# Optimization experiments

Hardware: AMD Instinct MI355X
Metric: run time of the kernel (lower is better)

## Reference

```python
import jax, jax.numpy as jnp
import numpy as np

N_IN = 128
N_BASIS = 16


def setup_inputs() -> dict:
    key = jax.random.key(0)
    ks = jax.random.split(key, 6)
    N, P = 50000, 200000
    prop = jax.random.normal(ks[0], (N, N_IN), dtype=jnp.float32)
    idx_i = jax.random.randint(ks[1], (P,), 0, N, dtype=jnp.int64)
    idx_j = jax.random.randint(ks[2], (P,), 0, N, dtype=jnp.int64)
    basis = jax.random.normal(ks[3], (P, N_BASIS), dtype=jnp.float32)
    # bias-free MLP: n_in=128 -> hidden 256 (tanh) -> n_out=2048
    W1 = jax.random.normal(ks[4], (N_IN, 256), dtype=jnp.float32) * (1.0 / np.sqrt(N_IN))
    W2 = jax.random.normal(ks[5], (256, N_IN * N_BASIS), dtype=jnp.float32) * (1.0 / np.sqrt(256))
    return {"prop": prop, "idx_i": idx_i, "idx_j": idx_j, "basis": basis, "W1": W1, "W2": W2}


def reference(prop, idx_i, idx_j, basis, W1, W2):
    # gather node features at edge endpoints and sum
    inter = prop[idx_i] + prop[idx_j]              # [P, n_in]
    # bias-free MLP with tanh on hidden layer
    h = jnp.tanh(inter @ W1)                       # [P, 256]
    h = h @ W2                                     # [P, n_in * n_basis]
    # contract with per-edge basis: 'pcb,pb->pc'
    h = h.reshape(-1, N_IN, N_BASIS)               # [P, n_in, n_basis]
    out = jnp.einsum('pcb,pb->pc', h, basis)       # [P, n_in]
    return out[:, None, :]                         # [P, 1, n_in]
```

## Files before the change

kernel.cpp:

```cpp
#include <hip/hip_runtime.h>

#define N_IN 128
#define HID 256
#define NB 16
#define BM 128
#define HS_STRIDE 264
#define BS_STRIDE 17

typedef __attribute__((ext_vector_type(8))) short s8v;
typedef __attribute__((ext_vector_type(4))) float f4v;

__device__ __forceinline__ unsigned short f2bf(float f) {
  unsigned int u = __float_as_uint(f);
  u += 0x7fffu + ((u >> 16) & 1u);
  return (unsigned short)(u >> 16);
}

__device__ __forceinline__ float tanh_fast(float x) {
  float e = __expf(2.0f * x);
  return 1.0f - 2.0f * __builtin_amdgcn_rcpf(e + 1.0f);
}

__global__ void __launch_bounds__(256)
prep2_kernel(const float* __restrict__ W1, const float* __restrict__ W2,
             unsigned short* __restrict__ W1f, unsigned short* __restrict__ W2f) {
  __shared__ unsigned short T[32 * 1024];

  const int t = threadIdx.x;
  const int lane = t & 63;
  const int wv = t >> 6;
  const int l15 = lane & 15;
  const int l4 = lane >> 4;
  const int bid = blockIdx.x;

  if (bid < 16) {
    const int kk = bid >> 1, ch = bid & 1;
    const float* src = W2 + (long)(kk * 32) * (N_IN * NB) + ch * 1024;
#pragma unroll
    for (int it = 0; it < 32; ++it) {
      int idx = it * 256 + t;
      int r = idx >> 8;
      int c4 = idx & 255;
      f4v v = __builtin_nontemporal_load((const f4v*)(src + r * (N_IN * NB) + c4 * 4));
      unsigned short* d = &T[r * 1024 + c4 * 4];
      d[0] = f2bf(v[0]); d[1] = f2bf(v[1]); d[2] = f2bf(v[2]); d[3] = f2bf(v[3]);
    }
    __syncthreads();
#pragma unroll
    for (int fi = 0; fi < 16; ++fi) {
      int f = fi * 4 + wv;
      int b = f >> 2, ctl = f & 3;
      int colb = ctl * 256 + l15 * 16 + b;
      s8v v;
#pragma unroll
      for (int j = 0; j < 8; ++j)
        v[j] = (short)T[(l4 * 8 + j) * 1024 + colb];
      *(s8v*)(W2f + ((((b * 8 + kk) * 8 + (ch * 4 + ctl)) * 64 + lane) << 3)) = v;
    }
  } else if (bid < 20) {
    const int kk = bid - 16;
    const float* src = W1 + (long)(kk * 32) * HID;
#pragma unroll
    for (int it = 0; it < 8; ++it) {
      int idx = it * 256 + t;
      int r = idx >> 6;
      int c4 = idx & 63;
      f4v v = __builtin_nontemporal_load((const f4v*)(src + r * HID + c4 * 4));
      unsigned short* d = &T[r * 256 + c4 * 4];
      d[0] = f2bf(v[0]); d[1] = f2bf(v[1]); d[2] = f2bf(v[2]); d[3] = f2bf(v[3]);
    }
    __syncthreads();
#pragma unroll
    for (int fi = 0; fi < 4; ++fi) {
      int f = fi * 4 + wv;
      int pass = f >> 3, ct = f & 7;
      int col = pass * 128 + ct * 16 + l15;
      s8v v;
#pragma unroll
      for (int j = 0; j < 8; ++j)
        v[j] = (short)T[(l4 * 8 + j) * 256 + col];
      *(s8v*)(W1f + ((((pass * 4 + kk) * 8 + ct) * 64 + lane) << 3)) = v;
    }
  }
}

__global__ void __launch_bounds__(256, 2)
pilayer_kernel(const float* __restrict__ prop,
               const int* __restrict__ idx_i,
               const int* __restrict__ idx_j,
               const float* __restrict__ basis,
               const unsigned short* __restrict__ W1f,
               const unsigned short* __restrict__ W2f,
               float* __restrict__ out, int P) {
  __shared__ unsigned short Hs[BM * HS_STRIDE];
  __shared__ float basisS[BM * BS_STRIDE];

  const int t = threadIdx.x;
  const int lane = t & 63;
  const int wv = t >> 6;
  const int l15 = lane & 15;
  const int l4 = lane >> 4;
  const int tile0 = blockIdx.x * BM;
  const int row0 = wv * 32;

  int pidx[2], qidx[2];
#pragma unroll
  for (int rt = 0; rt < 2; ++rt) {
    int p = tile0 + row0 + rt * 16 + l15; if (p >= P) p = P - 1;
    pidx[rt] = idx_i[p];
    qidx[rt] = idx_j[p];
  }

  {
    int r = t >> 1;
    int c0 = (t & 1) * 8;
    int p = tile0 + r; if (p >= P) p = P - 1;
    const f4v* bp = (const f4v*)(basis + (long)p * NB + c0);
    f4v b0 = __builtin_nontemporal_load(bp);
    f4v b1 = __builtin_nontemporal_load(bp + 1);
    float* dst = &basisS[r * BS_STRIDE + c0];
    dst[0] = b0[0]; dst[1] = b0[1]; dst[2] = b0[2]; dst[3] = b0[3];
    dst[4] = b1[0]; dst[5] = b1[1]; dst[6] = b1[2]; dst[7] = b1[3];
  }

  {
    s8v afr[4][2];
#pragma unroll
    for (int kk = 0; kk < 4; ++kk) {
      int k0 = kk * 32 + l4 * 8;
#pragma unroll
      for (int rt = 0; rt < 2; ++rt) {
        const float4* ai = (const float4*)(prop + (long)pidx[rt] * N_IN + k0);
        const float4* aj = (const float4*)(prop + (long)qidx[rt] * N_IN + k0);
        float4 x0 = ai[0], x1 = ai[1];
        float4 y0 = aj[0], y1 = aj[1];
        s8v a;
        a[0] = (short)f2bf(x0.x + y0.x); a[1] = (short)f2bf(x0.y + y0.y);
        a[2] = (short)f2bf(x0.z + y0.z); a[3] = (short)f2bf(x0.w + y0.w);
        a[4] = (short)f2bf(x1.x + y1.x); a[5] = (short)f2bf(x1.y + y1.y);
        a[6] = (short)f2bf(x1.z + y1.z); a[7] = (short)f2bf(x1.w + y1.w);
        afr[kk][rt] = a;
      }
    }
#pragma unroll
    for (int pass = 0; pass < 2; ++pass) {
      f4v acc[2][8];
#pragma unroll
      for (int rt = 0; rt < 2; ++rt)
#pragma unroll
        for (int ct = 0; ct < 8; ++ct) acc[rt][ct] = (f4v){0.f, 0.f, 0.f, 0.f};
#pragma unroll
      for (int kk = 0; kk < 4; ++kk) {
#pragma unroll
        for (int ct = 0; ct < 8; ++ct) {
          s8v bfr = *(const s8v*)(W1f + ((((pass * 4 + kk) * 8 + ct) * 64 + lane) << 3));
#pragma unroll
          for (int rt = 0; rt < 2; ++rt)
            acc[rt][ct] = __builtin_amdgcn_mfma_f32_16x16x32_bf16(afr[kk][rt], bfr, acc[rt][ct], 0, 0, 0);
        }
      }
#pragma unroll
      for (int rt = 0; rt < 2; ++rt)
#pragma unroll
        for (int ct = 0; ct < 8; ++ct)
#pragma unroll
          for (int r = 0; r < 4; ++r) {
            int lrow = row0 + rt * 16 + l4 * 4 + r;
            int col = pass * 128 + ct * 16 + l15;
            Hs[lrow * HS_STRIDE + col] = f2bf(tanh_fast(acc[rt][ct][r]));
          }
    }
  }

  __syncthreads();

  const int rg = wv >> 1, cg = wv & 1;
  const int rbase = rg * 64;

  f4v o[4][4];
#pragma unroll
  for (int rt = 0; rt < 4; ++rt)
#pragma unroll
    for (int q = 0; q < 4; ++q) o[rt][q] = (f4v){0.f, 0.f, 0.f, 0.f};

#pragma unroll 1
  for (int khalf = 0; khalf < 2; ++khalf) {
    s8v areg[4][4];
#pragma unroll
    for (int rt = 0; rt < 4; ++rt)
#pragma unroll
      for (int kloc = 0; kloc < 4; ++kloc)
        areg[rt][kloc] = *(const s8v*)&Hs[(rbase + rt * 16 + l15) * HS_STRIDE +
                                          (khalf * 4 + kloc) * 32 + l4 * 8];

    s8v bf[4][4];
#pragma unroll
    for (int q0 = 0; q0 < 3; ++q0)
#pragma unroll
      for (int kloc = 0; kloc < 4; ++kloc)
        bf[q0][kloc] = *(const s8v*)(W2f +
            ((((khalf * 4 + kloc) * 8) + cg * 4 + q0) << 9) + lane * 8);

#pragma unroll 1
    for (int b = 0; b < 16; ++b) {
      float bs[4][4];
#pragma unroll
      for (int rt = 0; rt < 4; ++rt)
#pragma unroll
        for (int r = 0; r < 4; ++r)
          bs[rt][r] = basisS[(rbase + rt * 16 + l4 * 4 + r) * BS_STRIDE + b];

#pragma unroll
      for (int q = 0; q < 4; ++q) {
        {
          int nb = b + ((q + 3) >> 2); if (nb > 15) nb = 15;
          int nq = (q + 3) & 3;
#pragma unroll
          for (int kloc = 0; kloc < 4; ++kloc)
            bf[(q + 3) & 3][kloc] = *(const s8v*)(W2f +
                (((nb * 8 + khalf * 4 + kloc) * 8 + cg * 4 + nq) << 9) + lane * 8);
        }
        f4v g[4];
#pragma unroll
        for (int rt = 0; rt < 4; ++rt) g[rt] = (f4v){0.f, 0.f, 0.f, 0.f};
        __builtin_amdgcn_s_setprio(1);
#pragma unroll
        for (int kloc = 0; kloc < 4; ++kloc)
#pragma unroll
          for (int rt = 0; rt < 4; ++rt)
            g[rt] = __builtin_amdgcn_mfma_f32_16x16x32_bf16(areg[rt][kloc], bf[q][kloc], g[rt], 0, 0, 0);
        __builtin_amdgcn_s_setprio(0);
#pragma unroll
        for (int rt = 0; rt < 4; ++rt)
#pragma unroll
          for (int r = 0; r < 4; ++r)
            o[rt][q][r] += g[rt][r] * bs[rt][r];
      }
    }
  }

#pragma unroll
  for (int rt = 0; rt < 4; ++rt)
#pragma unroll
    for (int r = 0; r < 4; ++r) {
      int p = tile0 + rbase + rt * 16 + l4 * 4 + r;
      if (p < P) {
        float* op = out + (long)p * N_IN + cg * 64 + l15;
#pragma unroll
        for (int q = 0; q < 4; ++q)
          __builtin_nontemporal_store(o[rt][q][r], op + q * 16);
      }
    }
}

extern "C" void kernel_launch(void* const* d_in, const int* in_sizes, int n_in,
                              void* d_out, int out_size, void* d_ws, size_t ws_size,
                              hipStream_t stream) {
  const float* prop  = (const float*)d_in[0];
  const int* idx_i   = (const int*)d_in[1];
  const int* idx_j   = (const int*)d_in[2];
  const float* basis = (const float*)d_in[3];
  const float* W1    = (const float*)d_in[4];
  const float* W2    = (const float*)d_in[5];
  float* out = (float*)d_out;
  int P = in_sizes[1];

  unsigned short* W1f = (unsigned short*)d_ws;
  unsigned short* W2f = W1f + N_IN * HID;

  prep2_kernel<<<20, 256, 0, stream>>>(W1, W2, W1f, W2f);

  int ntiles = (P + BM - 1) / BM;
  pilayer_kernel<<<ntiles, 256, 0, stream>>>(prop, idx_i, idx_j, basis, W1f, W2f, out, P);
}
```

Before: 336.6 us.

## Switch second GEMM to 32x32x16 MFMA with repacked W2 and transposed basis

```diff
diff --git a/kernel.cpp b/kernel.cpp
--- a/kernel.cpp
+++ b/kernel.cpp
@@ -5,10 +5,10 @@
 #define NB 16
 #define BM 128
 #define HS_STRIDE 264
-#define BS_STRIDE 17
 
 typedef __attribute__((ext_vector_type(8))) short s8v;
 typedef __attribute__((ext_vector_type(4))) float f4v;
+typedef __attribute__((ext_vector_type(16))) float f16v;
 
 __device__ __forceinline__ unsigned short f2bf(float f) {
   unsigned int u = __float_as_uint(f);
@@ -22,43 +22,43 @@
 }
 
 __global__ void __launch_bounds__(256)
-prep2_kernel(const float* __restrict__ W1, const float* __restrict__ W2,
+prep4_kernel(const float* __restrict__ W1, const float* __restrict__ W2,
              unsigned short* __restrict__ W1f, unsigned short* __restrict__ W2f) {
-  __shared__ unsigned short T[32 * 1024];
+  __shared__ unsigned short T[8192];
 
   const int t = threadIdx.x;
   const int lane = t & 63;
   const int wv = t >> 6;
   const int l15 = lane & 15;
-  const int l4 = lane >> 4;
+  const int l31 = lane & 31;
+  const int l4 = (lane >> 4) & 3;
+  const int hi = lane >> 5;
   const int bid = blockIdx.x;
 
-  if (bid < 16) {
-    const int kk = bid >> 1, ch = bid & 1;
-    const float* src = W2 + (long)(kk * 32) * (N_IN * NB) + ch * 1024;
-#pragma unroll
-    for (int it = 0; it < 32; ++it) {
+  if (bid < 64) {
+    const int ks = bid >> 2, CT = bid & 3;
+    const float* src = W2 + (long)(ks * 16) * (N_IN * NB) + CT * 512;
+#pragma unroll
+    for (int it = 0; it < 8; ++it) {
       int idx = it * 256 + t;
-      int r = idx >> 8;
-      int c4 = idx & 255;
+      int r = idx >> 7;
+      int c4 = idx & 127;
       f4v v = __builtin_nontemporal_load((const f4v*)(src + r * (N_IN * NB) + c4 * 4));
-      unsigned short* d = &T[r * 1024 + c4 * 4];
+      unsigned short* d = &T[r * 512 + c4 * 4];
       d[0] = f2bf(v[0]); d[1] = f2bf(v[1]); d[2] = f2bf(v[2]); d[3] = f2bf(v[3]);
     }
     __syncthreads();
 #pragma unroll
-    for (int fi = 0; fi < 16; ++fi) {
-      int f = fi * 4 + wv;
-      int b = f >> 2, ctl = f & 3;
-      int colb = ctl * 256 + l15 * 16 + b;
+    for (int fi = 0; fi < 4; ++fi) {
+      int b = fi * 4 + wv;
       s8v v;
 #pragma unroll
       for (int j = 0; j < 8; ++j)
-        v[j] = (short)T[(l4 * 8 + j) * 1024 + colb];
-      *(s8v*)(W2f + ((((b * 8 + kk) * 8 + (ch * 4 + ctl)) * 64 + lane) << 3)) = v;
-    }
-  } else if (bid < 20) {
-    const int kk = bid - 16;
+        v[j] = (short)T[(hi * 8 + j) * 512 + l31 * 16 + b];
+      *(s8v*)(W2f + ((((b * 16 + ks) * 4 + CT) * 64 + lane) << 3)) = v;
+    }
+  } else if (bid < 68) {
+    const int kk = bid - 64;
     const float* src = W1 + (long)(kk * 32) * HID;
 #pragma unroll
     for (int it = 0; it < 8; ++it) {
@@ -93,13 +93,15 @@
                const unsigned short* __restrict__ W2f,
                float* __restrict__ out, int P) {
   __shared__ unsigned short Hs[BM * HS_STRIDE];
-  __shared__ float basisS[BM * BS_STRIDE];
+  __shared__ float basisT[NB * BM];
 
   const int t = threadIdx.x;
   const int lane = t & 63;
   const int wv = t >> 6;
   const int l15 = lane & 15;
-  const int l4 = lane >> 4;
+  const int l31 = lane & 31;
+  const int l4 = (lane >> 4) & 3;
+  const int hi = lane >> 5;
   const int tile0 = blockIdx.x * BM;
   const int row0 = wv * 32;
 
@@ -118,9 +120,11 @@
     const f4v* bp = (const f4v*)(basis + (long)p * NB + c0);
     f4v b0 = __builtin_nontemporal_load(bp);
     f4v b1 = __builtin_nontemporal_load(bp + 1);
-    float* dst = &basisS[r * BS_STRIDE + c0];
-    dst[0] = b0[0]; dst[1] = b0[1]; dst[2] = b0[2]; dst[3] = b0[3];
-    dst[4] = b1[0]; dst[5] = b1[1]; dst[6] = b1[2]; dst[7] = b1[3];
+#pragma unroll
+    for (int u = 0; u < 4; ++u) {
+      basisT[(c0 + u) * BM + r] = b0[u];
+      basisT[(c0 + 4 + u) * BM + r] = b1[u];
+    }
   }
 
   {
@@ -177,78 +181,89 @@
   const int rg = wv >> 1, cg = wv & 1;
   const int rbase = rg * 64;
 
-  f4v o[4][4];
-#pragma unroll
-  for (int rt = 0; rt < 4; ++rt)
-#pragma unroll
-    for (int q = 0; q < 4; ++q) o[rt][q] = (f4v){0.f, 0.f, 0.f, 0.f};
+  f16v o[2][2];
+#pragma unroll
+  for (int rt2 = 0; rt2 < 2; ++rt2)
+#pragma unroll
+    for (int ct = 0; ct < 2; ++ct)
+#pragma unroll
+      for (int e = 0; e < 16; ++e) o[rt2][ct][e] = 0.f;
+
+  s8v bf[2][4];
 
 #pragma unroll 1
   for (int khalf = 0; khalf < 2; ++khalf) {
-    s8v areg[4][4];
-#pragma unroll
-    for (int rt = 0; rt < 4; ++rt)
-#pragma unroll
-      for (int kloc = 0; kloc < 4; ++kloc)
-        areg[rt][kloc] = *(const s8v*)&Hs[(rbase + rt * 16 + l15) * HS_STRIDE +
-                                          (khalf * 4 + kloc) * 32 + l4 * 8];
-
-    s8v bf[4][4];
-#pragma unroll
-    for (int q0 = 0; q0 < 3; ++q0)
-#pragma unroll
-      for (int kloc = 0; kloc < 4; ++kloc)
-        bf[q0][kloc] = *(const s8v*)(W2f +
-            ((((khalf * 4 + kloc) * 8) + cg * 4 + q0) << 9) + lane * 8);
+    s8v areg[2][8];
+#pragma unroll
+    for (int rt2 = 0; rt2 < 2; ++rt2)
+#pragma unroll
+      for (int ksl = 0; ksl < 8; ++ksl)
+        areg[rt2][ksl] = *(const s8v*)&Hs[(rbase + rt2 * 32 + l31) * HS_STRIDE +
+                                          khalf * 128 + ksl * 16 + hi * 8];
+
+#pragma unroll
+    for (int kl = 0; kl < 4; ++kl) {
+      int ks = khalf * 8 + kl;
+      bf[0][kl] = *(const s8v*)(W2f + ((((0 * 16 + ks) * 4 + cg * 2 + 0) * 64 + lane) << 3));
+    }
 
 #pragma unroll 1
     for (int b = 0; b < 16; ++b) {
-      float bs[4][4];
-#pragma unroll
-      for (int rt = 0; rt < 4; ++rt)
-#pragma unroll
-        for (int r = 0; r < 4; ++r)
-          bs[rt][r] = basisS[(rbase + rt * 16 + l4 * 4 + r) * BS_STRIDE + b];
-
-#pragma unroll
-      for (int q = 0; q < 4; ++q) {
-        {
-          int nb = b + ((q + 3) >> 2); if (nb > 15) nb = 15;
-          int nq = (q + 3) & 3;
-#pragma unroll
-          for (int kloc = 0; kloc < 4; ++kloc)
-            bf[(q + 3) & 3][kloc] = *(const s8v*)(W2f +
-                (((nb * 8 + khalf * 4 + kloc) * 8 + cg * 4 + nq) << 9) + lane * 8);
+      f4v bsv[2][4];
+#pragma unroll
+      for (int rt2 = 0; rt2 < 2; ++rt2)
+#pragma unroll
+        for (int q4 = 0; q4 < 4; ++q4)
+          bsv[rt2][q4] = *(const f4v*)&basisT[b * BM + rbase + rt2 * 32 + q4 * 8 + hi * 4];
+
+#pragma unroll
+      for (int ct = 0; ct < 2; ++ct) {
+        f16v g[2];
+#pragma unroll
+        for (int rt2 = 0; rt2 < 2; ++rt2)
+#pragma unroll
+          for (int e = 0; e < 16; ++e) g[rt2][e] = 0.f;
+
+#pragma unroll
+        for (int kc = 0; kc < 2; ++kc) {
+          {
+            int nb = b, nct = ct, nkc = kc ^ 1;
+            if (kc == 1) { nct = ct ^ 1; if (ct == 1) { nb = b + 1; if (nb > 15) nb = 15; } nkc = 0; }
+#pragma unroll
+            for (int kl = 0; kl < 4; ++kl) {
+              int ks = khalf * 8 + nkc * 4 + kl;
+              bf[kc ^ 1][kl] = *(const s8v*)(W2f +
+                  ((((nb * 16 + ks) * 4 + cg * 2 + nct) * 64 + lane) << 3));
+            }
+          }
+          __builtin_amdgcn_s_setprio(1);
+#pragma unroll
+          for (int kl = 0; kl < 4; ++kl)
+#pragma unroll
+            for (int rt2 = 0; rt2 < 2; ++rt2)
+              g[rt2] = __builtin_amdgcn_mfma_f32_32x32x16_bf16(areg[rt2][kc * 4 + kl],
+                                                               bf[kc][kl], g[rt2], 0, 0, 0);
+          __builtin_amdgcn_s_setprio(0);
         }
-        f4v g[4];
-#pragma unroll
-        for (int rt = 0; rt < 4; ++rt) g[rt] = (f4v){0.f, 0.f, 0.f, 0.f};
-        __builtin_amdgcn_s_setprio(1);
-#pragma unroll
-        for (int kloc = 0; kloc < 4; ++kloc)
-#pragma unroll
-          for (int rt = 0; rt < 4; ++rt)
-            g[rt] = __builtin_amdgcn_mfma_f32_16x16x32_bf16(areg[rt][kloc], bf[q][kloc], g[rt], 0, 0, 0);
-        __builtin_amdgcn_s_setprio(0);
-#pragma unroll
-        for (int rt = 0; rt < 4; ++rt)
-#pragma unroll
-          for (int r = 0; r < 4; ++r)
-            o[rt][q][r] += g[rt][r] * bs[rt][r];
-      }
-    }
-  }
-
-#pragma unroll
-  for (int rt = 0; rt < 4; ++rt)
-#pragma unroll
-    for (int r = 0; r < 4; ++r) {
-      int p = tile0 + rbase + rt * 16 + l4 * 4 + r;
+#pragma unroll
+        for (int rt2 = 0; rt2 < 2; ++rt2)
+#pragma unroll
+          for (int reg = 0; reg < 16; ++reg)
+            o[rt2][ct][reg] += g[rt2][reg] * bsv[rt2][reg >> 2][reg & 3];
+      }
+    }
+  }
+
+#pragma unroll
+  for (int rt2 = 0; rt2 < 2; ++rt2)
+#pragma unroll
+    for (int reg = 0; reg < 16; ++reg) {
+      int p = tile0 + rbase + rt2 * 32 + (reg & 3) + 8 * (reg >> 2) + 4 * hi;
       if (p < P) {
-        float* op = out + (long)p * N_IN + cg * 64 + l15;
-#pragma unroll
-        for (int q = 0; q < 4; ++q)
-          __builtin_nontemporal_store(o[rt][q][r], op + q * 16);
+        float* op = out + (long)p * N_IN + cg * 64 + l31;
+#pragma unroll
+        for (int ct = 0; ct < 2; ++ct)
+          __builtin_nontemporal_store(o[rt2][ct][reg], op + ct * 32);
       }
     }
 }
@@ -268,7 +283,7 @@
   unsigned short* W1f = (unsigned short*)d_ws;
   unsigned short* W2f = W1f + N_IN * HID;
 
-  prep2_kernel<<<20, 256, 0, stream>>>(W1, W2, W1f, W2f);
+  prep4_kernel<<<68, 256, 0, stream>>>(W1, W2, W1f, W2f);
 
   int ntiles = (P + BM - 1) / BM;
   pilayer_kernel<<<ntiles, 256, 0, stream>>>(prop, idx_i, idx_j, basis, W1f, W2f, out, P);
```

Result: slower. 377.6 us (+12.2%).
